# Performance work log

Hardware: AMD Instinct MI355X
Metric: run time of the kernel (lower is better)

## Reference

```python
import jax, jax.numpy as jnp
import numpy as np

K = 3  # local attention window (kernel_size)


def setup_inputs() -> dict:
    key = jax.random.key(0)
    ks = jax.random.split(key, 10)
    B, C, S = 1, 128, 24
    scale = 1.0 / np.sqrt(C).astype(np.float32)
    x = jax.random.normal(ks[0], (B, C, S, S, S), dtype=jnp.float32)
    wq = jax.random.normal(ks[1], (C, C), dtype=jnp.float32) * scale
    bq = jax.random.normal(ks[2], (C,), dtype=jnp.float32) * 0.01
    wk = jax.random.normal(ks[3], (C, C), dtype=jnp.float32) * scale
    bk = jax.random.normal(ks[4], (C,), dtype=jnp.float32) * 0.01
    wv = jax.random.normal(ks[5], (C, C), dtype=jnp.float32) * scale
    bv = jax.random.normal(ks[6], (C,), dtype=jnp.float32) * 0.01
    rel_h = jax.random.normal(ks[7], (C // 2, K, 1, 1), dtype=jnp.float32)
    rel_w = jax.random.normal(ks[8], (C // 2, 1, K, 1), dtype=jnp.float32)
    rel_d = jax.random.normal(ks[9], (C // 2, 1, 1, K), dtype=jnp.float32)
    return {"x": x, "wq": wq, "bq": bq, "wk": wk, "bk": bk,
            "wv": wv, "bv": bv, "rel_h": rel_h, "rel_w": rel_w, "rel_d": rel_d}


def reference(x, wq, bq, wk, bk, wv, bv, rel_h, rel_w, rel_d):
    B, C, H, W, D = x.shape
    p = (K - 1) // 2
    pad = ((0, 0), (0, 0), (p, K - 1 - p), (p, K - 1 - p), (p, K - 1 - p))
    xp = jnp.pad(x, pad)

    # 1x1x1 Conv3d == per-voxel linear map
    conv1 = lambda y, w, b: jnp.einsum('bchwd,oc->bohwd', y, w) + b[None, :, None, None, None]
    q = conv1(x, wq, bq)          # [B,C,H,W,D]
    kf = conv1(xp, wk, bk)        # padded
    vf = conv1(xp, wv, bv)

    def unfold(y):
        # torch unfold(2,K,1).unfold(3,K,1).unfold(4,K,1) flattened row-major (i,j,l)
        pats = [y[:, :, i:i + H, j:j + W, l:l + D]
                for i in range(K) for j in range(K) for l in range(K)]
        return jnp.stack(pats, axis=-1)  # [B,C,H,W,D,K^3]

    kw = unfold(kf)
    vw = unfold(vf)

    # q^T k per voxel over the K^3 window (num_heads=1 so head split is identity)
    qk = jnp.einsum('bchwd,bchwds->bhwds', q, kw)  # [B,H,W,D,27]

    # Faithful to einsum('bhxytdz,cijk->bhxytijk'): d,z,c are all summed
    # independently -> (sum_d q) * (sum_c rel) broadcast over the window.
    qsum = jnp.sum(q, axis=1)                         # [B,H,W,D]
    bias = rel_h.sum(0) + rel_w.sum(0) + rel_d.sum(0)  # [K,K,K] via broadcast
    qk = qk.reshape(B, H, W, D, K, K, K) + qsum[..., None, None, None] * bias

    attn = jax.nn.softmax(qk.reshape(B, H, W, D, K ** 3), axis=-1)
    out = jnp.einsum('bhwds,bchwds->bhwdc', attn, vw)  # [B,H,W,D,C]
    # torch: [B,1,H,W,D,1,C].reshape(B,-1,H,W,D) -- same row-major flatten here
    return out.reshape(B, -1, H, W, D)
```

## Files before the change

### kernel.cpp

```cpp
#include <hip/hip_runtime.h>

#define CCH 128
#define SV 24
#define NVOX 13824

typedef unsigned short u16;
typedef unsigned int   u32;

__device__ __forceinline__ u16 f2bf(float f) {
    u32 x = __float_as_uint(f);
    u32 r = x + 0x7fffu + ((x >> 16) & 1u);
    return (u16)(r >> 16);
}
__device__ __forceinline__ void cvt8(uint4 r, float* f) {
    f[0] = __uint_as_float(r.x << 16); f[1] = __uint_as_float(r.x & 0xffff0000u);
    f[2] = __uint_as_float(r.y << 16); f[3] = __uint_as_float(r.y & 0xffff0000u);
    f[4] = __uint_as_float(r.z << 16); f[5] = __uint_as_float(r.z & 0xffff0000u);
    f[6] = __uint_as_float(r.w << 16); f[7] = __uint_as_float(r.w & 0xffff0000u);
}

__global__ __launch_bounds__(256) void proj_kernel(
    const float* __restrict__ x,
    const float* __restrict__ wq, const float* __restrict__ bq,
    const float* __restrict__ wk, const float* __restrict__ bk,
    const float* __restrict__ wv, const float* __restrict__ bv,
    const float* __restrict__ relh, const float* __restrict__ relw,
    const float* __restrict__ reld,
    float* __restrict__ qout, u16* __restrict__ kws, u16* __restrict__ vws,
    float* __restrict__ biasW)
{
    const int m = blockIdx.y;
    const float* __restrict__ w = (m == 0) ? wq : (m == 1) ? wk : wv;
    const float* __restrict__ b = (m == 0) ? bq : (m == 1) ? bk : bv;

    __shared__ float Xs[32][64];
    __shared__ float Ws[32][128];

    const int tid  = threadIdx.x;
    const int vox0 = blockIdx.x * 64;
    const int v0   = (tid & 15) * 4;
    const int o0   = (tid >> 4) * 8;

    const int xc  = tid >> 3;
    const int xv  = (tid & 7) * 4;
    const int wo  = tid >> 1;
    const int wkh = (tid & 1) * 16;

    float acc[4][8] = {{0.f}};

    for (int k0 = 0; k0 < CCH; k0 += 32) {
        {
            const float* src = x + (size_t)(k0 + xc) * NVOX + vox0 + xv;
            const float4 a0 = *(const float4*)src;
            const float4 a1 = *(const float4*)(src + 32);
            *(float4*)&Xs[xc][xv]      = a0;
            *(float4*)&Xs[xc][xv + 32] = a1;
        }
        {
            const float* src = w + (size_t)wo * CCH + k0 + wkh;
            const float4 b0 = *(const float4*)src;
            const float4 b1 = *(const float4*)(src + 4);
            const float4 b2 = *(const float4*)(src + 8);
            const float4 b3 = *(const float4*)(src + 12);
            Ws[wkh + 0][wo] = b0.x;  Ws[wkh + 1][wo] = b0.y;
            Ws[wkh + 2][wo] = b0.z;  Ws[wkh + 3][wo] = b0.w;
            Ws[wkh + 4][wo] = b1.x;  Ws[wkh + 5][wo] = b1.y;
            Ws[wkh + 6][wo] = b1.z;  Ws[wkh + 7][wo] = b1.w;
            Ws[wkh + 8][wo] = b2.x;  Ws[wkh + 9][wo] = b2.y;
            Ws[wkh + 10][wo] = b2.z; Ws[wkh + 11][wo] = b2.w;
            Ws[wkh + 12][wo] = b3.x; Ws[wkh + 13][wo] = b3.y;
            Ws[wkh + 14][wo] = b3.z; Ws[wkh + 15][wo] = b3.w;
        }
        __syncthreads();

#pragma unroll
        for (int k = 0; k < 32; ++k) {
            const float4 xf = *(const float4*)&Xs[k][v0];
            const float4 w0 = *(const float4*)&Ws[k][o0];
            const float4 w1 = *(const float4*)&Ws[k][o0 + 4];
            const float xr[4] = {xf.x, xf.y, xf.z, xf.w};
            const float wr[8] = {w0.x, w0.y, w0.z, w0.w,
                                 w1.x, w1.y, w1.z, w1.w};
#pragma unroll
            for (int vv = 0; vv < 4; ++vv)
#pragma unroll
                for (int oo = 0; oo < 8; ++oo)
                    acc[vv][oo] = fmaf(xr[vv], wr[oo], acc[vv][oo]);
        }
        __syncthreads();
    }

    const float4 bf0 = *(const float4*)(b + o0);
    const float4 bf1 = *(const float4*)(b + o0 + 4);
    const float br[8] = {bf0.x, bf0.y, bf0.z, bf0.w,
                         bf1.x, bf1.y, bf1.z, bf1.w};

#pragma unroll
    for (int vv = 0; vv < 4; ++vv) {
        float r[8];
#pragma unroll
        for (int oo = 0; oo < 8; ++oo) r[oo] = acc[vv][oo] + br[oo];
        const size_t row = (size_t)(vox0 + v0 + vv) * CCH + o0;
        if (m == 0) {
            float4 s0 = {r[0], r[1], r[2], r[3]};
            float4 s1 = {r[4], r[5], r[6], r[7]};
            *(float4*)(qout + row) = s0;
            *(float4*)(qout + row + 4) = s1;
        } else {
            u16* out = (m == 1) ? kws : vws;
            uint4 st;
            st.x = (u32)f2bf(r[0]) | ((u32)f2bf(r[1]) << 16);
            st.y = (u32)f2bf(r[2]) | ((u32)f2bf(r[3]) << 16);
            st.z = (u32)f2bf(r[4]) | ((u32)f2bf(r[5]) << 16);
            st.w = (u32)f2bf(r[6]) | ((u32)f2bf(r[7]) << 16);
            *(uint4*)(out + row) = st;
        }
    }

    if (blockIdx.x == 0) {
        if (m == 1 && tid < CCH) kws[(size_t)NVOX * CCH + tid] = f2bf(bk[tid]);
        if (m == 2 && tid < CCH) vws[(size_t)NVOX * CCH + tid] = f2bf(bv[tid]);
        if (m == 1 && tid < 27) {
            const int i = tid / 9, j = (tid / 3) % 3, l = tid % 3;
            float s = 0.f;
            for (int c = 0; c < 64; ++c)
                s += relh[c * 3 + i] + relw[c * 3 + j] + reld[c * 3 + l];
            biasW[tid] = s;
        }
    }
}

__device__ __forceinline__ int nbr_off(int h, int w, int d, int s, int ch) {
    const int nh = h + s / 9 - 1;
    const int nw = w + (s / 3) % 3 - 1;
    const int nd = d + s % 3 - 1;
    const bool ok = ((unsigned)nh < (unsigned)SV) &&
                    ((unsigned)nw < (unsigned)SV) &&
                    ((unsigned)nd < (unsigned)SV);
    const int idx = ok ? ((nh * SV + nw) * SV + nd) : NVOX;
    return idx * CCH + ch;
}

__global__ __launch_bounds__(256) void attn_kernel(
    float* __restrict__ qo, const u16* __restrict__ kws,
    const u16* __restrict__ vws, const float* __restrict__ biasW)
{
    const int tid  = threadIdx.x;
    const int lane = tid & 15;
    const int vox  = blockIdx.x * 16 + (tid >> 4);
    const int h    = vox / 576;
    const int rem  = vox - h * 576;
    const int w    = rem / 24;
    const int d    = rem - w * 24;
    const int ch   = lane * 8;

    const float* qrow = qo + (size_t)vox * CCH + ch;
    const float4 q0 = *(const float4*)qrow;
    const float4 q1 = *(const float4*)(qrow + 4);
    const float qr[8] = {q0.x, q0.y, q0.z, q0.w, q1.x, q1.y, q1.z, q1.w};

    float qs = qr[0] + qr[1] + qr[2] + qr[3] + qr[4] + qr[5] + qr[6] + qr[7];
#pragma unroll
    for (int mm = 1; mm < 16; mm <<= 1) qs += __shfl_xor(qs, mm, 64);

    float ps[27];
#pragma unroll
    for (int sb = 0; sb < 27; sb += 9) {
        uint4 kf[9];
#pragma unroll
        for (int j = 0; j < 9; ++j)
            kf[j] = *(const uint4*)(kws + nbr_off(h, w, d, sb + j, ch));
#pragma unroll
        for (int j = 0; j < 9; ++j) {
            float f[8];
            cvt8(kf[j], f);
            float p = qr[0] * f[0];
            p = fmaf(qr[1], f[1], p); p = fmaf(qr[2], f[2], p);
            p = fmaf(qr[3], f[3], p); p = fmaf(qr[4], f[4], p);
            p = fmaf(qr[5], f[5], p); p = fmaf(qr[6], f[6], p);
            p = fmaf(qr[7], f[7], p);
            ps[sb + j] = p;
        }
    }

#pragma unroll
    for (int mm = 1; mm < 16; mm <<= 1) {
#pragma unroll
        for (int s = 0; s < 27; ++s) ps[s] += __shfl_xor(ps[s], mm, 64);
    }

#pragma unroll
    for (int s = 0; s < 27; ++s) ps[s] = fmaf(qs, biasW[s], ps[s]);

    float mx = ps[0];
#pragma unroll
    for (int s = 1; s < 27; ++s) mx = fmaxf(mx, ps[s]);
    float sum = 0.f;
#pragma unroll
    for (int s = 0; s < 27; ++s) { ps[s] = __expf(ps[s] - mx); sum += ps[s]; }
    const float inv = 1.f / sum;
#pragma unroll
    for (int s = 0; s < 27; ++s) ps[s] *= inv;

    float o[8] = {0.f, 0.f, 0.f, 0.f, 0.f, 0.f, 0.f, 0.f};
#pragma unroll
    for (int sb = 0; sb < 27; sb += 9) {
        uint4 vf[9];
#pragma unroll
        for (int j = 0; j < 9; ++j)
            vf[j] = *(const uint4*)(vws + nbr_off(h, w, d, sb + j, ch));
#pragma unroll
        for (int j = 0; j < 9; ++j) {
            float f[8];
            cvt8(vf[j], f);
            const float a = ps[sb + j];
#pragma unroll
            for (int e = 0; e < 8; ++e) o[e] = fmaf(a, f[e], o[e]);
        }
    }

    float* dst = qo + (size_t)vox * CCH + ch;
    float4 s0 = {o[0], o[1], o[2], o[3]};
    float4 s1 = {o[4], o[5], o[6], o[7]};
    *(float4*)dst = s0;
    *(float4*)(dst + 4) = s1;
}

extern "C" void kernel_launch(void* const* d_in, const int* in_sizes, int n_in,
                              void* d_out, int out_size, void* d_ws,
                              size_t ws_size, hipStream_t stream)
{
    const float* x    = (const float*)d_in[0];
    const float* wq   = (const float*)d_in[1];
    const float* bq   = (const float*)d_in[2];
    const float* wk   = (const float*)d_in[3];
    const float* bk   = (const float*)d_in[4];
    const float* wv   = (const float*)d_in[5];
    const float* bv   = (const float*)d_in[6];
    const float* relh = (const float*)d_in[7];
    const float* relw = (const float*)d_in[8];
    const float* reld = (const float*)d_in[9];

    u16*   kws   = (u16*)d_ws;
    u16*   vws   = kws + (size_t)(NVOX + 1) * CCH;
    float* biasW = (float*)(vws + (size_t)(NVOX + 1) * CCH);

    dim3 pgrid(NVOX / 64, 3);
    proj_kernel<<<pgrid, 256, 0, stream>>>(x, wq, bq, wk, bk, wv, bv,
                                           relh, relw, reld,
                                           (float*)d_out, kws, vws, biasW);
    attn_kernel<<<NVOX / 16, 256, 0, stream>>>((float*)d_out, kws, vws, biasW);
}
```

Baseline: 109.3 us.

## Split projection over output halves, store K in fp32, widen attention lanes per voxel

The projection kernel gains a z grid dimension that splits the output channels into two 64-wide halves. This doubles the block count and shrinks per-thread accumulators from 32 to 16, at the cost of reading x twice. K is now stored in fp32 instead of bf16, which removes conversion work but doubles K gather traffic. The attention kernel uses 32 lanes per voxel with 4 channels each instead of 16 lanes with 8, which doubles the blocks and adds one more shuffle-reduction stage across the 27 scores.

New measurement: 115.1 us. 1.05x slower.

```diff
diff --git a/kernel.cpp b/kernel.cpp
--- a/kernel.cpp
+++ b/kernel.cpp
@@ -12,11 +12,9 @@
     u32 r = x + 0x7fffu + ((x >> 16) & 1u);
     return (u16)(r >> 16);
 }
-__device__ __forceinline__ void cvt8(uint4 r, float* f) {
+__device__ __forceinline__ void cvt4b(uint2 r, float* f) {
     f[0] = __uint_as_float(r.x << 16); f[1] = __uint_as_float(r.x & 0xffff0000u);
     f[2] = __uint_as_float(r.y << 16); f[3] = __uint_as_float(r.y & 0xffff0000u);
-    f[4] = __uint_as_float(r.z << 16); f[5] = __uint_as_float(r.z & 0xffff0000u);
-    f[6] = __uint_as_float(r.w << 16); f[7] = __uint_as_float(r.w & 0xffff0000u);
 }
 
 __global__ __launch_bounds__(256) void proj_kernel(
@@ -26,7 +24,7 @@
     const float* __restrict__ wv, const float* __restrict__ bv,
     const float* __restrict__ relh, const float* __restrict__ relw,
     const float* __restrict__ reld,
-    float* __restrict__ qout, u16* __restrict__ kws, u16* __restrict__ vws,
+    float* __restrict__ qout, float* __restrict__ kws, u16* __restrict__ vws,
     float* __restrict__ biasW)
 {
     const int m = blockIdx.y;
@@ -34,19 +32,20 @@
     const float* __restrict__ b = (m == 0) ? bq : (m == 1) ? bk : bv;
 
     __shared__ float Xs[32][64];
-    __shared__ float Ws[32][128];
+    __shared__ float Ws[32][64];
 
     const int tid  = threadIdx.x;
     const int vox0 = blockIdx.x * 64;
+    const int oblk = blockIdx.z * 64;
     const int v0   = (tid & 15) * 4;
-    const int o0   = (tid >> 4) * 8;
+    const int o0   = (tid >> 4) * 4;
 
     const int xc  = tid >> 3;
     const int xv  = (tid & 7) * 4;
-    const int wo  = tid >> 1;
-    const int wkh = (tid & 1) * 16;
-
-    float acc[4][8] = {{0.f}};
+    const int wo  = tid & 63;
+    const int wkh = (tid >> 6) * 8;
+
+    float acc[4][4] = {{0.f}};
 
     for (int k0 = 0; k0 < CCH; k0 += 32) {
         {
@@ -57,68 +56,56 @@
             *(float4*)&Xs[xc][xv + 32] = a1;
         }
         {
-            const float* src = w + (size_t)wo * CCH + k0 + wkh;
+            const float* src = w + (size_t)(oblk + wo) * CCH + k0 + wkh;
             const float4 b0 = *(const float4*)src;
             const float4 b1 = *(const float4*)(src + 4);
-            const float4 b2 = *(const float4*)(src + 8);
-            const float4 b3 = *(const float4*)(src + 12);
-            Ws[wkh + 0][wo] = b0.x;  Ws[wkh + 1][wo] = b0.y;
-            Ws[wkh + 2][wo] = b0.z;  Ws[wkh + 3][wo] = b0.w;
-            Ws[wkh + 4][wo] = b1.x;  Ws[wkh + 5][wo] = b1.y;
-            Ws[wkh + 6][wo] = b1.z;  Ws[wkh + 7][wo] = b1.w;
-            Ws[wkh + 8][wo] = b2.x;  Ws[wkh + 9][wo] = b2.y;
-            Ws[wkh + 10][wo] = b2.z; Ws[wkh + 11][wo] = b2.w;
-            Ws[wkh + 12][wo] = b3.x; Ws[wkh + 13][wo] = b3.y;
-            Ws[wkh + 14][wo] = b3.z; Ws[wkh + 15][wo] = b3.w;
+            Ws[wkh + 0][wo] = b0.x; Ws[wkh + 1][wo] = b0.y;
+            Ws[wkh + 2][wo] = b0.z; Ws[wkh + 3][wo] = b0.w;
+            Ws[wkh + 4][wo] = b1.x; Ws[wkh + 5][wo] = b1.y;
+            Ws[wkh + 6][wo] = b1.z; Ws[wkh + 7][wo] = b1.w;
         }
         __syncthreads();
 
 #pragma unroll
         for (int k = 0; k < 32; ++k) {
             const float4 xf = *(const float4*)&Xs[k][v0];
-            const float4 w0 = *(const float4*)&Ws[k][o0];
-            const float4 w1 = *(const float4*)&Ws[k][o0 + 4];
+            const float4 wf = *(const float4*)&Ws[k][o0];
             const float xr[4] = {xf.x, xf.y, xf.z, xf.w};
-            const float wr[8] = {w0.x, w0.y, w0.z, w0.w,
-                                 w1.x, w1.y, w1.z, w1.w};
+            const float wr[4] = {wf.x, wf.y, wf.z, wf.w};
 #pragma unroll
             for (int vv = 0; vv < 4; ++vv)
 #pragma unroll
-                for (int oo = 0; oo < 8; ++oo)
+                for (int oo = 0; oo < 4; ++oo)
                     acc[vv][oo] = fmaf(xr[vv], wr[oo], acc[vv][oo]);
         }
         __syncthreads();
     }
 
-    const float4 bf0 = *(const float4*)(b + o0);
-    const float4 bf1 = *(const float4*)(b + o0 + 4);
-    const float br[8] = {bf0.x, bf0.y, bf0.z, bf0.w,
-                         bf1.x, bf1.y, bf1.z, bf1.w};
+    const float4 bf = *(const float4*)(b + oblk + o0);
+    const float br[4] = {bf.x, bf.y, bf.z, bf.w};
 
 #pragma unroll
     for (int vv = 0; vv < 4; ++vv) {
-        float r[8];
-#pragma unroll
-        for (int oo = 0; oo < 8; ++oo) r[oo] = acc[vv][oo] + br[oo];
-        const size_t row = (size_t)(vox0 + v0 + vv) * CCH + o0;
+        float r[4];
+#pragma unroll
+        for (int oo = 0; oo < 4; ++oo) r[oo] = acc[vv][oo] + br[oo];
+        const size_t row = (size_t)(vox0 + v0 + vv) * CCH + oblk + o0;
         if (m == 0) {
-            float4 s0 = {r[0], r[1], r[2], r[3]};
-            float4 s1 = {r[4], r[5], r[6], r[7]};
-            *(float4*)(qout + row) = s0;
-            *(float4*)(qout + row + 4) = s1;
+            float4 st = {r[0], r[1], r[2], r[3]};
+            *(float4*)(qout + row) = st;
+        } else if (m == 1) {
+            float4 st = {r[0], r[1], r[2], r[3]};
+            *(float4*)(kws + row) = st;
         } else {
-            u16* out = (m == 1) ? kws : vws;
-            uint4 st;
+            uint2 st;
             st.x = (u32)f2bf(r[0]) | ((u32)f2bf(r[1]) << 16);
             st.y = (u32)f2bf(r[2]) | ((u32)f2bf(r[3]) << 16);
-            st.z = (u32)f2bf(r[4]) | ((u32)f2bf(r[5]) << 16);
-            st.w = (u32)f2bf(r[6]) | ((u32)f2bf(r[7]) << 16);
-            *(uint4*)(out + row) = st;
-        }
-    }
-
-    if (blockIdx.x == 0) {
-        if (m == 1 && tid < CCH) kws[(size_t)NVOX * CCH + tid] = f2bf(bk[tid]);
+            *(uint2*)(vws + row) = st;
+        }
+    }
+
+    if (blockIdx.x == 0 && blockIdx.z == 0) {
+        if (m == 1 && tid < CCH) kws[(size_t)NVOX * CCH + tid] = bk[tid];
         if (m == 2 && tid < CCH) vws[(size_t)NVOX * CCH + tid] = f2bf(bv[tid]);
         if (m == 1 && tid < 27) {
             const int i = tid / 9, j = (tid / 3) % 3, l = tid % 3;
@@ -142,49 +129,44 @@
 }
 
 __global__ __launch_bounds__(256) void attn_kernel(
-    float* __restrict__ qo, const u16* __restrict__ kws,
+    float* __restrict__ qo, const float* __restrict__ kws,
     const u16* __restrict__ vws, const float* __restrict__ biasW)
 {
     const int tid  = threadIdx.x;
-    const int lane = tid & 15;
-    const int vox  = blockIdx.x * 16 + (tid >> 4);
+    const int lane = tid & 31;
+    const int vox  = blockIdx.x * 8 + (tid >> 5);
     const int h    = vox / 576;
     const int rem  = vox - h * 576;
     const int w    = rem / 24;
     const int d    = rem - w * 24;
-    const int ch   = lane * 8;
-
-    const float* qrow = qo + (size_t)vox * CCH + ch;
-    const float4 q0 = *(const float4*)qrow;
-    const float4 q1 = *(const float4*)(qrow + 4);
-    const float qr[8] = {q0.x, q0.y, q0.z, q0.w, q1.x, q1.y, q1.z, q1.w};
-
-    float qs = qr[0] + qr[1] + qr[2] + qr[3] + qr[4] + qr[5] + qr[6] + qr[7];
-#pragma unroll
-    for (int mm = 1; mm < 16; mm <<= 1) qs += __shfl_xor(qs, mm, 64);
+    const int ch   = lane * 4;
+
+    const float4 q4 = *(const float4*)(qo + (size_t)vox * CCH + ch);
+    const float qr[4] = {q4.x, q4.y, q4.z, q4.w};
+
+    float qs = qr[0] + qr[1] + qr[2] + qr[3];
+#pragma unroll
+    for (int mm = 1; mm < 32; mm <<= 1) qs += __shfl_xor(qs, mm, 64);
 
     float ps[27];
 #pragma unroll
     for (int sb = 0; sb < 27; sb += 9) {
-        uint4 kf[9];
+        float4 kf[9];
 #pragma unroll
         for (int j = 0; j < 9; ++j)
-            kf[j] = *(const uint4*)(kws + nbr_off(h, w, d, sb + j, ch));
+            kf[j] = *(const float4*)(kws + nbr_off(h, w, d, sb + j, ch));
 #pragma unroll
         for (int j = 0; j < 9; ++j) {
-            float f[8];
-            cvt8(kf[j], f);
-            float p = qr[0] * f[0];
-            p = fmaf(qr[1], f[1], p); p = fmaf(qr[2], f[2], p);
-            p = fmaf(qr[3], f[3], p); p = fmaf(qr[4], f[4], p);
-            p = fmaf(qr[5], f[5], p); p = fmaf(qr[6], f[6], p);
-            p = fmaf(qr[7], f[7], p);
+            float p = qr[0] * kf[j].x;
+            p = fmaf(qr[1], kf[j].y, p);
+            p = fmaf(qr[2], kf[j].z, p);
+            p = fmaf(qr[3], kf[j].w, p);
             ps[sb + j] = p;
         }
     }
 
 #pragma unroll
-    for (int mm = 1; mm < 16; mm <<= 1) {
+    for (int mm = 1; mm < 32; mm <<= 1) {
 #pragma unroll
         for (int s = 0; s < 27; ++s) ps[s] += __shfl_xor(ps[s], mm, 64);
     }
@@ -202,28 +184,25 @@
 #pragma unroll
     for (int s = 0; s < 27; ++s) ps[s] *= inv;
 
-    float o[8] = {0.f, 0.f, 0.f, 0.f, 0.f, 0.f, 0.f, 0.f};
+    float o[4] = {0.f, 0.f, 0.f, 0.f};
 #pragma unroll
     for (int sb = 0; sb < 27; sb += 9) {
-        uint4 vf[9];
+        uint2 vf[9];
 #pragma unroll
         for (int j = 0; j < 9; ++j)
-            vf[j] = *(const uint4*)(vws + nbr_off(h, w, d, sb + j, ch));
+            vf[j] = *(const uint2*)(vws + nbr_off(h, w, d, sb + j, ch));
 #pragma unroll
         for (int j = 0; j < 9; ++j) {
-            float f[8];
-            cvt8(vf[j], f);
+            float f[4];
+            cvt4b(vf[j], f);
             const float a = ps[sb + j];
-#pragma unroll
-            for (int e = 0; e < 8; ++e) o[e] = fmaf(a, f[e], o[e]);
-        }
-    }
-
-    float* dst = qo + (size_t)vox * CCH + ch;
-    float4 s0 = {o[0], o[1], o[2], o[3]};
-    float4 s1 = {o[4], o[5], o[6], o[7]};
-    *(float4*)dst = s0;
-    *(float4*)(dst + 4) = s1;
+            o[0] = fmaf(a, f[0], o[0]); o[1] = fmaf(a, f[1], o[1]);
+            o[2] = fmaf(a, f[2], o[2]); o[3] = fmaf(a, f[3], o[3]);
+        }
+    }
+
+    float4 st = {o[0], o[1], o[2], o[3]};
+    *(float4*)(qo + (size_t)vox * CCH + ch) = st;
 }
 
 extern "C" void kernel_launch(void* const* d_in, const int* in_sizes, int n_in,
@@ -241,13 +220,13 @@
     const float* relw = (const float*)d_in[8];
     const float* reld = (const float*)d_in[9];
 
-    u16*   kws   = (u16*)d_ws;
-    u16*   vws   = kws + (size_t)(NVOX + 1) * CCH;
+    float* kws   = (float*)d_ws;
+    u16*   vws   = (u16*)(kws + (size_t)(NVOX + 1) * CCH);
     float* biasW = (float*)(vws + (size_t)(NVOX + 1) * CCH);
 
-    dim3 pgrid(NVOX / 64, 3);
+    dim3 pgrid(NVOX / 64, 3, 2);
     proj_kernel<<<pgrid, 256, 0, stream>>>(x, wq, bq, wk, bk, wv, bv,
                                            relh, relw, reld,
                                            (float*)d_out, kws, vws, biasW);
-    attn_kernel<<<NVOX / 16, 256, 0, stream>>>((float*)d_out, kws, vws, biasW);
-}
+    attn_kernel<<<NVOX / 8, 256, 0, stream>>>((float*)d_out, kws, vws, biasW);
+}
```
